# Kernel tuning notes

Hardware: AMD Instinct MI355X
Metric: run time of the kernel (lower is better)

The kernel has to match this reference:

```python
import jax, jax.numpy as jnp
import numpy as np

N = 50000
F_IN = 128
E = 800000
C = 32      # hidden_channels
H1 = 8      # heads_1
H2 = 1      # heads_2
NEG_SLOPE = 0.2


def setup_inputs() -> dict:
    key = jax.random.key(0)
    ks = jax.random.split(key, 16)
    s = 0.1
    x = jax.random.normal(ks[0], (N, F_IN), dtype=jnp.float32)
    edge_index = jax.random.randint(ks[1], (2, E), 0, N, dtype=jnp.int32)
    # layer 1: in=F_IN, out=C, heads=H1, concat=True
    Wl1 = jax.random.normal(ks[2], (H1 * C, F_IN), dtype=jnp.float32) * s
    bl1 = jnp.zeros((H1 * C,), dtype=jnp.float32)
    Wr1 = jax.random.normal(ks[3], (H1 * C, F_IN), dtype=jnp.float32) * s
    br1 = jnp.zeros((H1 * C,), dtype=jnp.float32)
    att1 = jax.random.normal(ks[4], (H1, C), dtype=jnp.float32) * s
    bias1 = jnp.zeros((H1 * C,), dtype=jnp.float32)
    # layer 2: in=H1*C, out=C, heads=H2, concat=False (mean)
    Wl2 = jax.random.normal(ks[5], (H2 * C, H1 * C), dtype=jnp.float32) * s
    bl2 = jnp.zeros((H2 * C,), dtype=jnp.float32)
    Wr2 = jax.random.normal(ks[6], (H2 * C, H1 * C), dtype=jnp.float32) * s
    br2 = jnp.zeros((H2 * C,), dtype=jnp.float32)
    att2 = jax.random.normal(ks[7], (H2, C), dtype=jnp.float32) * s
    bias2 = jnp.zeros((C,), dtype=jnp.float32)
    return {"x": x, "edge_index": edge_index,
            "Wl1": Wl1, "bl1": bl1, "Wr1": Wr1, "br1": br1, "att1": att1, "bias1": bias1,
            "Wl2": Wl2, "bl2": bl2, "Wr2": Wr2, "br2": br2, "att2": att2, "bias2": bias2}


def _gatv2_layer(x, src, dst, Wl, bl, Wr, br, att, bias, heads, out_c, concat):
    n = x.shape[0]
    xl = (x @ Wl.T + bl).reshape(n, heads, out_c)  # source transform
    xr = (x @ Wr.T + br).reshape(n, heads, out_c)  # target transform
    z = jax.nn.leaky_relu(xl[src] + xr[dst], NEG_SLOPE)          # [E, H, C]
    logit = jnp.einsum('ehc,hc->eh', z, att)                     # [E, H]
    # segment softmax over incoming edges of each target node
    m = jax.ops.segment_max(logit, dst, num_segments=n)          # [N, H]
    ex = jnp.exp(logit - m[dst])
    denom = jax.ops.segment_sum(ex, dst, num_segments=n)
    alpha = ex / jnp.maximum(denom[dst], 1e-16)                  # [E, H]
    out = jax.ops.segment_sum(alpha[..., None] * xl[src], dst, num_segments=n)  # [N, H, C]
    out = out.reshape(n, heads * out_c) if concat else out.mean(axis=1)
    return out + bias


def reference(x, edge_index, Wl1, bl1, Wr1, br1, att1, bias1,
              Wl2, bl2, Wr2, br2, att2, bias2):
    n = x.shape[0]
    # PyG GATv2Conv default: add self loops
    loops = jnp.arange(n, dtype=edge_index.dtype)
    src = jnp.concatenate([edge_index[0], loops])
    dst = jnp.concatenate([edge_index[1], loops])
    h = _gatv2_layer(x, src, dst, Wl1, bl1, Wr1, br1, att1, bias1, H1, C, True)
    h = jax.nn.gelu(h, approximate=False)
    out = _gatv2_layer(h, src, dst, Wl2, bl2, Wr2, br2, att2, bias2, H2, C, False)
    return out
```

## Files before the change

kernel.cpp:

```cpp
#include <hip/hip_runtime.h>
#include <hip/hip_bf16.h>


typedef unsigned short u16;
typedef short bf16x8 __attribute__((ext_vector_type(8)));
typedef float f32x4 __attribute__((ext_vector_type(4)));
typedef float f32x2 __attribute__((ext_vector_type(2)));

#define F_IN   128
#define CH     32
#define H1     8
#define JT1    512
#define JH1    256
#define JT2    64
#define JH2    32

#define OFF_Y1     0UL
#define OFF_H      52000000UL
#define OFF_Y2     78000000UL
#define OFF_COL    85000000UL
#define OFF_DEG    89000000UL
#define OFF_ROW    89400000UL
#define OFF_CUR    89800000UL
#define OFF_WC     90200000UL
#define OFF_FLAG   90600000UL
#define OFF_BSUM   90700000UL
#define WS_NEED    91000000UL

#define W_WL1   0
#define W_BL1   32768
#define W_WR1   33024
#define W_BR1   65792
#define W_ATT1  66048
#define W_BIAS1 66304
#define W_WL2   66560
#define W_BL2   74752
#define W_WR2   74784
#define W_BR2   82976
#define W_ATT2  83008
#define W_BIAS2 83040
#define W_TOTAL 83072

__device__ inline float b2f(u16 u) { return __uint_as_float(((unsigned)u) << 16); }
__device__ inline u16 f2b(float f) {
    unsigned u = __float_as_uint(f);
    unsigned r = (u + 0x7fffu + ((u >> 16) & 1u)) >> 16;
    return (u16)r;
}
__device__ inline unsigned cvtpk(float lo, float hi) {
    unsigned r;
    asm("v_cvt_pk_bf16_f32 %0, %1, %2" : "=v"(r) : "v"(lo), "v"(hi));
    return r;
}
__device__ inline f32x2 pk_add(f32x2 a, f32x2 b) {
    f32x2 d;
    asm("v_pk_add_f32 %0, %1, %2" : "=v"(d) : "v"(a), "v"(b));
    return d;
}
__device__ inline f32x2 pk_mul(f32x2 a, f32x2 b) {
    f32x2 d;
    asm("v_pk_mul_f32 %0, %1, %2" : "=v"(d) : "v"(a), "v"(b));
    return d;
}
__device__ inline f32x2 pk_fma(f32x2 a, f32x2 b, f32x2 c) {
    f32x2 d;
    asm("v_pk_fma_f32 %0, %1, %2, %3" : "=v"(d) : "v"(a), "v"(b), "v"(c));
    return d;
}
__device__ inline f32x2 unpk(unsigned u) {
    f32x2 d;
    d.x = __uint_as_float(u << 16);
    d.y = __uint_as_float(u & 0xffff0000u);
    return d;
}
__device__ inline f32x2 pabs(f32x2 z) {
    f32x2 d;
    d.x = __uint_as_float(__float_as_uint(z.x) & 0x7fffffffu);
    d.y = __uint_as_float(__float_as_uint(z.y) & 0x7fffffffu);
    return d;
}

struct WcArgs { const void* src[12]; int cum[13]; };

__global__ __launch_bounds__(256) void prep(
    WcArgs a, const u16* __restrict__ xprobe, u16* __restrict__ dst, int total,
    int* __restrict__ flagOut, int NBW,
    const int* __restrict__ ei, int* __restrict__ deg, int E_, int NP) {
    const int t = threadIdx.x;
    if ((int)blockIdx.x >= NBW) {
        int e = ((int)blockIdx.x - NBW) * 256 + t;
        if (e >= E_ + NP) return;
        int dstn = (e < E_) ? ei[E_ + e] : e - E_;
        atomicAdd(deg + dstn, 1);
        return;
    }
    __shared__ int cnt[256];
    __shared__ int sflag;
    int c = 0;
    for (int i = t; i < 512; i += 256) {
        u16 u = xprobe[i];
        int e = (u >> 7) & 0xff;
        c += (u == 0 || (e >= 100 && e <= 141)) ? 1 : 0;
    }
    cnt[t] = c; __syncthreads();
    for (int off = 128; off; off >>= 1) {
        if (t < off) cnt[t] += cnt[t + off];
        __syncthreads();
    }
    if (t == 0) {
        sflag = (cnt[0] >= 440) ? 1 : 0;
        if (blockIdx.x == 0) *flagOut = sflag;
    }
    __syncthreads();
    const int fl = sflag;
    int i = blockIdx.x * 256 + t;
    if (i >= total) return;
    int s = 0;
    while (i >= a.cum[s + 1]) s++;
    int rel = i - a.cum[s];
    if (fl) dst[i] = ((const u16*)a.src[s])[rel];
    else    dst[i] = f2b(((const float*)a.src[s])[rel]);
}

__global__ __launch_bounds__(256) void scan_part(const int* __restrict__ deg,
                                                 int* __restrict__ bsum, int NN) {
    __shared__ int red[256];
    int b = blockIdx.x, t = threadIdx.x;
    int base = b * 1024 + t * 4;
    int s = 0;
#pragma unroll
    for (int j = 0; j < 4; j++) { int i = base + j; if (i < NN) s += deg[i]; }
    red[t] = s; __syncthreads();
    for (int off = 128; off; off >>= 1) {
        if (t < off) red[t] += red[t + off];
        __syncthreads();
    }
    if (t == 0) bsum[b] = red[0];
}

__global__ __launch_bounds__(256) void scan_final(
    const int* __restrict__ deg, const int* __restrict__ bsum,
    int* __restrict__ rowptr, int* __restrict__ cur, int NN, int NB) {
    __shared__ int sb[256];
    __shared__ int ps[256];
    int b = blockIdx.x, t = threadIdx.x;
    int bv = (t < NB) ? bsum[t] : 0;
    sb[t] = bv; __syncthreads();
    for (int off = 1; off < 256; off <<= 1) {
        int x = (t >= off) ? sb[t - off] : 0;
        __syncthreads();
        sb[t] += x;
        __syncthreads();
    }
    if (b == 0 && t == 0) rowptr[NN] = sb[NB - 1];
    int boff = (b == 0) ? 0 : sb[b - 1];

    int base = b * 1024 + t * 4;
    int v[4]; int s = 0;
#pragma unroll
    for (int j = 0; j < 4; j++) { int i = base + j; v[j] = (i < NN) ? deg[i] : 0; s += v[j]; }
    ps[t] = s; __syncthreads();
    for (int off = 1; off < 256; off <<= 1) {
        int x = (t >= off) ? ps[t - off] : 0;
        __syncthreads();
        ps[t] += x;
        __syncthreads();
    }
    int run = boff + (t ? ps[t - 1] : 0);
#pragma unroll
    for (int j = 0; j < 4; j++) {
        int i = base + j;
        if (i < NN) { rowptr[i] = run; cur[i] = run; run += v[j]; }
    }
}

template <int K, int NG, bool DYN>
__device__ __forceinline__ void gemm_body(
    float (*cs)[32][68],
    const void* __restrict__ X, const u16* __restrict__ Wl, const u16* __restrict__ Wr,
    const u16* __restrict__ bl, const u16* __restrict__ br,
    u16* __restrict__ Y, int M, int JH, const int* __restrict__ flagp, int bm0) {
    const int t = threadIdx.x, w = t >> 6, l = t & 63;
    const int JT = 2 * JH;
    const int lr = l & 15, lk = (l >> 4) * 8;
    const int fl = DYN ? *flagp : 1;

    int rowm[2];
#pragma unroll
    for (int mt = 0; mt < 2; mt++) {
        int row = bm0 + w * 32 + mt * 16 + lr;
        if (row >= M) row = M - 1;
        rowm[mt] = row;
    }

    constexpr int KK = K / 32;
    bf16x8 afr[2][KK];
    if (fl) {
        const u16* xb = (const u16*)X;
#pragma unroll
        for (int mt = 0; mt < 2; mt++)
#pragma unroll
            for (int kk = 0; kk < KK; kk++)
                afr[mt][kk] = *(const bf16x8*)(xb + (size_t)rowm[mt] * K + lk + kk * 32);
    } else {
        const float* xf = (const float*)X;
#pragma unroll
        for (int mt = 0; mt < 2; mt++)
#pragma unroll
            for (int kk = 0; kk < KK; kk++) {
                const float* p = xf + (size_t)rowm[mt] * K + lk + kk * 32;
                float4 v0 = *(const float4*)p;
                float4 v1 = *(const float4*)(p + 4);
                uint4 o;
                o.x = cvtpk(v0.x, v0.y); o.y = cvtpk(v0.z, v0.w);
                o.z = cvtpk(v1.x, v1.y); o.w = cvtpk(v1.z, v1.w);
                afr[mt][kk] = *(bf16x8*)&o;
            }
    }

#pragma unroll 1
    for (int g = 0; g < NG; g++) {
        const int bn0 = g * 64;
        const u16* bx[4];
        float bv[4];
#pragma unroll
        for (int nt = 0; nt < 4; nt++) {
            int j = bn0 + nt * 16 + lr;
            const u16* wp = (j < JH) ? (Wl + (size_t)j * K) : (Wr + (size_t)(j - JH) * K);
            bx[nt] = wp + lk;
            bv[nt] = b2f(j < JH ? bl[j] : br[j - JH]);
        }

        f32x4 acc[2][4];
#pragma unroll
        for (int mt = 0; mt < 2; mt++)
#pragma unroll
            for (int nt = 0; nt < 4; nt++) acc[mt][nt] = (f32x4){0.f, 0.f, 0.f, 0.f};

#pragma unroll
        for (int kk = 0; kk < KK; kk++) {
            bf16x8 b[4];
#pragma unroll
            for (int nt = 0; nt < 4; nt++) b[nt] = *(const bf16x8*)(bx[nt] + kk * 32);
#pragma unroll
            for (int mt = 0; mt < 2; mt++)
#pragma unroll
                for (int nt = 0; nt < 4; nt++)
                    acc[mt][nt] = __builtin_amdgcn_mfma_f32_16x16x32_bf16(
                        afr[mt][kk], b[nt], acc[mt][nt], 0, 0, 0);
        }

#pragma unroll
        for (int mt = 0; mt < 2; mt++)
#pragma unroll
            for (int nt = 0; nt < 4; nt++)
#pragma unroll
                for (int r = 0; r < 4; r++)
                    cs[w][mt * 16 + (l >> 4) * 4 + r][nt * 16 + lr] = acc[mt][nt][r] + bv[nt];

#pragma unroll
        for (int p = 0; p < 4; p++) {
            int rl = p * 8 + (l >> 3);
            int grow = bm0 + w * 32 + rl;
            if (grow < M) {
                const float* rp = &cs[w][rl][(l & 7) * 8];
                float4 v0 = *(const float4*)rp;
                float4 v1 = *(const float4*)(rp + 4);
                uint4 o;
                o.x = cvtpk(v0.x, v0.y); o.y = cvtpk(v0.z, v0.w);
                o.z = cvtpk(v1.x, v1.y); o.w = cvtpk(v1.z, v1.w);
                *(uint4*)(Y + (size_t)grow * JT + bn0 + (l & 7) * 8) = o;
            }
        }
    }
}

__global__ __launch_bounds__(256) void gemm1_scatter(
    const void* __restrict__ X, const u16* __restrict__ Wl, const u16* __restrict__ Wr,
    const u16* __restrict__ bl, const u16* __restrict__ br,
    u16* __restrict__ Y, int M, const int* __restrict__ flagp, int NBG,
    const int* __restrict__ ei, int* __restrict__ cur, int* __restrict__ col,
    int E_, int NP) {
    __shared__ float cs[4][32][68];
    if ((int)blockIdx.x < NBG) {
        gemm_body<F_IN, 8, true>(cs, X, Wl, Wr, bl, br, Y, M, JH1, flagp,
                                 (int)blockIdx.x * 128);
        return;
    }
    int e = ((int)blockIdx.x - NBG) * 256 + threadIdx.x;
    if (e >= E_ + NP) return;
    int src, dst;
    if (e < E_) { src = ei[e]; dst = ei[E_ + e]; }
    else        { src = dst = e - E_; }
    int pos = atomicAdd(cur + dst, 1);
    col[pos] = src;
}

__global__ __launch_bounds__(256) void gemm2_k(
    const u16* __restrict__ X, const u16* __restrict__ Wl, const u16* __restrict__ Wr,
    const u16* __restrict__ bl, const u16* __restrict__ br,
    u16* __restrict__ Y, int M, const int* __restrict__ flagp) {
    __shared__ float cs[4][32][68];
    gemm_body<JH1, 1, false>(cs, X, Wl, Wr, bl, br, Y, M, JH2, flagp,
                             (int)blockIdx.x * 128);
}

__global__ __launch_bounds__(256, 4) void agg1(
    const u16* __restrict__ Y1, const int* __restrict__ rowptr,
    const int* __restrict__ col, const u16* __restrict__ att,
    const u16* __restrict__ bias, u16* __restrict__ hout, int NN) {
    const int wid = blockIdx.x * 4 + (threadIdx.x >> 6);
    if (wid >= NN) return;
    const int lane = threadIdx.x & 63, half = lane >> 5, hl = lane & 31;
    const int n = wid;

    f32x2 xr2[4], a06[4], a04[4];
    {
        uint4 rx = *(const uint4*)(Y1 + (size_t)n * JT1 + JH1 + hl * 8);
        uint4 ra = *(const uint4*)(att + hl * 8);
        unsigned ux[4] = {rx.x, rx.y, rx.z, rx.w};
        unsigned ua[4] = {ra.x, ra.y, ra.z, ra.w};
#pragma unroll
        for (int p = 0; p < 4; p++) {
            xr2[p] = unpk(ux[p]);
            f32x2 a = unpk(ua[p]);
            a06[p].x = 0.6f * a.x; a06[p].y = 0.6f * a.y;
            a04[p].x = 0.4f * a.x; a04[p].y = 0.4f * a.y;
        }
    }
    f32x2 acc2[4] = {{0.f,0.f},{0.f,0.f},{0.f,0.f},{0.f,0.f}};
    float dsum = 0.f;

    auto edge = [&](uint4 raw) {
        unsigned uw[4] = {raw.x, raw.y, raw.z, raw.w};
        f32x2 xl2[4];
        f32x2 p2 = {0.f, 0.f};
#pragma unroll
        for (int p = 0; p < 4; p++) {
            xl2[p] = unpk(uw[p]);
            f32x2 z = pk_add(xl2[p], xr2[p]);
            p2 = pk_fma(z, a06[p], p2);
            p2 = pk_fma(pabs(z), a04[p], p2);
        }
        float pl = p2.x + p2.y;
        pl += __shfl_xor(pl, 1); pl += __shfl_xor(pl, 2);
        float e = __expf(pl);
        dsum += e;
        f32x2 e2; e2.x = e; e2.y = e;
#pragma unroll
        for (int p = 0; p < 4; p++) acc2[p] = pk_fma(e2, xl2[p], acc2[p]);
    };

    const int beg = rowptr[n], end = rowptr[n + 1];
    int i = beg + half;
    for (; i + 14 < end; i += 16) {
        int s[8];
#pragma unroll
        for (int k = 0; k < 8; k++) s[k] = col[i + 2 * k];
        uint4 r[8];
#pragma unroll
        for (int k = 0; k < 8; k++) r[k] = *(const uint4*)(Y1 + (size_t)s[k] * JT1 + hl * 8);
#pragma unroll
        for (int k = 0; k < 8; k++) edge(r[k]);
    }
    for (; i + 6 < end; i += 8) {
        int s0 = col[i], s1 = col[i + 2], s2 = col[i + 4], s3 = col[i + 6];
        uint4 r0 = *(const uint4*)(Y1 + (size_t)s0 * JT1 + hl * 8);
        uint4 r1 = *(const uint4*)(Y1 + (size_t)s1 * JT1 + hl * 8);
        uint4 r2 = *(const uint4*)(Y1 + (size_t)s2 * JT1 + hl * 8);
        uint4 r3 = *(const uint4*)(Y1 + (size_t)s3 * JT1 + hl * 8);
        edge(r0); edge(r1); edge(r2); edge(r3);
    }
    for (; i < end; i += 2) {
        uint4 r0 = *(const uint4*)(Y1 + (size_t)col[i] * JT1 + hl * 8);
        edge(r0);
    }

    dsum += __shfl_xor(dsum, 32);
#pragma unroll
    for (int p = 0; p < 4; p++) {
        acc2[p].x += __shfl_xor(acc2[p].x, 32);
        acc2[p].y += __shfl_xor(acc2[p].y, 32);
    }

    if (half == 0) {
        float inv = 1.f / fmaxf(dsum, 1e-16f);
        u16 bu[8];
        *(uint4*)bu = *(const uint4*)(bias + hl * 8);
        float v[8];
#pragma unroll
        for (int p = 0; p < 4; p++) {
            float x0 = acc2[p].x * inv + b2f(bu[2 * p]);
            float x1 = acc2[p].y * inv + b2f(bu[2 * p + 1]);
            v[2 * p]     = 0.5f * x0 * (1.f + erff(x0 * 0.70710678118654752f));
            v[2 * p + 1] = 0.5f * x1 * (1.f + erff(x1 * 0.70710678118654752f));
        }
        uint4 o;
        o.x = cvtpk(v[0], v[1]); o.y = cvtpk(v[2], v[3]);
        o.z = cvtpk(v[4], v[5]); o.w = cvtpk(v[6], v[7]);
        *(uint4*)(hout + (size_t)n * JH1 + hl * 8) = o;
    }
}

__global__ __launch_bounds__(256) void agg2(
    const u16* __restrict__ Y2, const int* __restrict__ rowptr,
    const int* __restrict__ col, const u16* __restrict__ att,
    const u16* __restrict__ bias, void* __restrict__ dout, int NN,
    const int* __restrict__ flag) {
    const int wid = blockIdx.x * 4 + (threadIdx.x >> 6);
    if (wid >= NN) return;
    const int lane = threadIdx.x & 63, le = lane >> 4, cl = lane & 15;
    const int n = wid;

    f32x2 xr2 = unpk(*(const unsigned*)(Y2 + (size_t)n * JT2 + JH2 + cl * 2));
    f32x2 av  = unpk(*(const unsigned*)(att + cl * 2));
    f32x2 a06; a06.x = 0.6f * av.x; a06.y = 0.6f * av.y;
    f32x2 a04; a04.x = 0.4f * av.x; a04.y = 0.4f * av.y;
    f32x2 acc2 = {0.f, 0.f};
    float dsum = 0.f;

    auto edge = [&](unsigned raw, bool act) {
        f32x2 xl2 = unpk(raw);
        f32x2 z = pk_add(xl2, xr2);
        f32x2 p2 = pk_fma(z, a06, (f32x2){0.f, 0.f});
        p2 = pk_fma(pabs(z), a04, p2);
        float pl = p2.x + p2.y;
        pl += __shfl_xor(pl, 1); pl += __shfl_xor(pl, 2);
        pl += __shfl_xor(pl, 4); pl += __shfl_xor(pl, 8);
        float e = __expf(pl);
        if (!act) e = 0.f;
        dsum += e;
        f32x2 e2; e2.x = e; e2.y = e;
        acc2 = pk_fma(e2, xl2, acc2);
    };

    const int beg = rowptr[n], end = rowptr[n + 1];
    int i = beg;
    for (; i + 16 <= end; i += 16) {
        int s0 = col[i + le], s1 = col[i + 4 + le];
        int s2 = col[i + 8 + le], s3 = col[i + 12 + le];
        unsigned r0 = *(const unsigned*)(Y2 + (size_t)s0 * JT2 + cl * 2);
        unsigned r1 = *(const unsigned*)(Y2 + (size_t)s1 * JT2 + cl * 2);
        unsigned r2 = *(const unsigned*)(Y2 + (size_t)s2 * JT2 + cl * 2);
        unsigned r3 = *(const unsigned*)(Y2 + (size_t)s3 * JT2 + cl * 2);
        edge(r0, true); edge(r1, true); edge(r2, true); edge(r3, true);
    }
    for (; i + 8 <= end; i += 8) {
        int sA = col[i + le];
        int sB = col[i + 4 + le];
        unsigned rA = *(const unsigned*)(Y2 + (size_t)sA * JT2 + cl * 2);
        unsigned rB = *(const unsigned*)(Y2 + (size_t)sB * JT2 + cl * 2);
        edge(rA, true);
        edge(rB, true);
    }
    for (; i < end; i += 4) {
        int idx = i + le;
        bool act = idx < end;
        int s0 = col[act ? idx : end - 1];
        unsigned r0 = *(const unsigned*)(Y2 + (size_t)s0 * JT2 + cl * 2);
        edge(r0, act);
    }

    dsum += __shfl_xor(dsum, 16); dsum += __shfl_xor(dsum, 32);
    acc2.x += __shfl_xor(acc2.x, 16); acc2.x += __shfl_xor(acc2.x, 32);
    acc2.y += __shfl_xor(acc2.y, 16); acc2.y += __shfl_xor(acc2.y, 32);

    if (le == 0) {
        float inv = 1.f / fmaxf(dsum, 1e-16f);
        f32x2 bv = unpk(*(const unsigned*)(bias + cl * 2));
        float v0 = acc2.x * inv + bv.x;
        float v1 = acc2.y * inv + bv.y;
        if (*flag) {
            *(unsigned*)((u16*)dout + n * JH2 + cl * 2) = cvtpk(v0, v1);
        } else {
            float2 o; o.x = v0; o.y = v1;
            *(float2*)((float*)dout + n * JH2 + cl * 2) = o;
        }
    }
}

extern "C" void kernel_launch(void* const* d_in, const int* in_sizes, int n_in,
                              void* d_out, int out_size, void* d_ws, size_t ws_size,
                              hipStream_t stream) {
    const int NN = in_sizes[0] / F_IN;
    const int EE = in_sizes[1] / 2;
    const int EP = EE + NN;
    if (ws_size < WS_NEED) return;

    char* w = (char*)d_ws;
    u16*   Y1   = (u16*)(w + OFF_Y1);
    u16*   hbuf = (u16*)(w + OFF_H);
    u16*   Y2   = (u16*)(w + OFF_Y2);
    int*   col  = (int*)(w + OFF_COL);
    int*   deg  = (int*)(w + OFF_DEG);
    int*   rowp = (int*)(w + OFF_ROW);
    int*   cur  = (int*)(w + OFF_CUR);
    u16*   Wc   = (u16*)(w + OFF_WC);
    int*   flag = (int*)(w + OFF_FLAG);
    int*   bsum = (int*)(w + OFF_BSUM);

    const int* ei = (const int*)d_in[1];

    hipMemsetAsync(deg, 0, (size_t)NN * 4, stream);
    {
        WcArgs a;
        int sizes[12] = {JH1 * F_IN, JH1, JH1 * F_IN, JH1, H1 * CH, JH1,
                         JH2 * JH1, JH2, JH2 * JH1, JH2, JH2, JH2};
        int c = 0;
        for (int s = 0; s < 12; s++) { a.src[s] = d_in[2 + s]; a.cum[s] = c; c += sizes[s]; }
        a.cum[12] = c;
        const int NBW = (W_TOTAL + 255) / 256;
        const int NBE = (EP + 255) / 256;
        prep<<<NBW + NBE, 256, 0, stream>>>(a, (const u16*)d_in[0], Wc, W_TOTAL,
                                            flag, NBW, ei, deg, EE, NN);
    }

    const int NB = (NN + 1023) / 1024;
    scan_part<<<NB, 256, 0, stream>>>(deg, bsum, NN);
    scan_final<<<NB, 256, 0, stream>>>(deg, bsum, rowp, cur, NN, NB);

    {
        const int NBG = (NN + 127) / 128;
        const int NBE = (EP + 255) / 256;
        gemm1_scatter<<<NBG + NBE, 256, 0, stream>>>(
            d_in[0], Wc + W_WL1, Wc + W_WR1, Wc + W_BL1, Wc + W_BR1,
            Y1, NN, flag, NBG, ei, cur, col, EE, NN);
    }
    agg1<<<(NN + 3) / 4, 256, 0, stream>>>(Y1, rowp, col, Wc + W_ATT1,
                                           Wc + W_BIAS1, hbuf, NN);

    gemm2_k<<<(NN + 127) / 128, 256, 0, stream>>>(
        hbuf, Wc + W_WL2, Wc + W_WR2, Wc + W_BL2, Wc + W_BR2, Y2, NN, flag);
    agg2<<<(NN + 3) / 4, 256, 0, stream>>>(Y2, rowp, col, Wc + W_ATT2,
                                           Wc + W_BIAS2, d_out, NN, flag);
}
```

Baseline: 242.0 us.

## Process nodes in degree-sorted order in aggregation kernels for load balance

Builds a histogram of node in-degrees during the scan and prefix-sums it. A new kernel scatters node ids into a degree-sorted permutation, which agg1 and agg2 use to map waves to nodes. The aim is to group nodes of similar in-degree into the same blocks and reduce imbalance from uneven edge counts. The cost is an extra kernel, atomics, and loss of contiguous node access for the self-feature reads and output writes.

```diff
diff --git a/kernel.cpp b/kernel.cpp
--- a/kernel.cpp
+++ b/kernel.cpp
@@ -19,7 +19,10 @@
 #define OFF_H      52000000UL
 #define OFF_Y2     78000000UL
 #define OFF_COL    85000000UL
+#define OFF_PERM   88400000UL
 #define OFF_DEG    89000000UL
+#define OFF_DH     89200000UL
+#define OFF_DCUR   89201024UL
 #define OFF_ROW    89400000UL
 #define OFF_CUR    89800000UL
 #define OFF_WC     90200000UL
@@ -123,24 +126,37 @@
 }
 
 __global__ __launch_bounds__(256) void scan_part(const int* __restrict__ deg,
-                                                 int* __restrict__ bsum, int NN) {
+                                                 int* __restrict__ bsum,
+                                                 int* __restrict__ dh, int NN) {
     __shared__ int red[256];
+    __shared__ int lh[256];
     int b = blockIdx.x, t = threadIdx.x;
+    lh[t] = 0;
     int base = b * 1024 + t * 4;
     int s = 0;
-#pragma unroll
-    for (int j = 0; j < 4; j++) { int i = base + j; if (i < NN) s += deg[i]; }
+    __syncthreads();
+#pragma unroll
+    for (int j = 0; j < 4; j++) {
+        int i = base + j;
+        if (i < NN) {
+            int v = deg[i];
+            s += v;
+            atomicAdd(&lh[v < 255 ? v : 255], 1);
+        }
+    }
     red[t] = s; __syncthreads();
     for (int off = 128; off; off >>= 1) {
         if (t < off) red[t] += red[t + off];
         __syncthreads();
     }
     if (t == 0) bsum[b] = red[0];
+    if (lh[t]) atomicAdd(dh + t, lh[t]);
 }
 
 __global__ __launch_bounds__(256) void scan_final(
     const int* __restrict__ deg, const int* __restrict__ bsum,
-    int* __restrict__ rowptr, int* __restrict__ cur, int NN, int NB) {
+    int* __restrict__ rowptr, int* __restrict__ cur, int NN, int NB,
+    const int* __restrict__ dh, int* __restrict__ dcur) {
     __shared__ int sb[256];
     __shared__ int ps[256];
     int b = blockIdx.x, t = threadIdx.x;
@@ -172,6 +188,28 @@
         int i = base + j;
         if (i < NN) { rowptr[i] = run; cur[i] = run; run += v[j]; }
     }
+
+    if (b == 0) {
+        __syncthreads();
+        int dv = dh[t];
+        sb[t] = dv; __syncthreads();
+        for (int off = 1; off < 256; off <<= 1) {
+            int x = (t >= off) ? sb[t - off] : 0;
+            __syncthreads();
+            sb[t] += x;
+            __syncthreads();
+        }
+        dcur[t] = sb[t] - dv;
+    }
+}
+
+__global__ void dsort_scatter(const int* __restrict__ deg, int* __restrict__ dcur,
+                              int* __restrict__ perm, int NN) {
+    int i = blockIdx.x * 256 + threadIdx.x;
+    if (i >= NN) return;
+    int v = deg[i];
+    int pos = atomicAdd(dcur + (v < 255 ? v : 255), 1);
+    perm[pos] = i;
 }
 
 template <int K, int NG, bool DYN>
@@ -308,11 +346,12 @@
 __global__ __launch_bounds__(256, 4) void agg1(
     const u16* __restrict__ Y1, const int* __restrict__ rowptr,
     const int* __restrict__ col, const u16* __restrict__ att,
-    const u16* __restrict__ bias, u16* __restrict__ hout, int NN) {
+    const u16* __restrict__ bias, u16* __restrict__ hout, int NN,
+    const int* __restrict__ perm) {
     const int wid = blockIdx.x * 4 + (threadIdx.x >> 6);
     if (wid >= NN) return;
     const int lane = threadIdx.x & 63, half = lane >> 5, hl = lane & 31;
-    const int n = wid;
+    const int n = perm[wid];
 
     f32x2 xr2[4], a06[4], a04[4];
     {
@@ -406,11 +445,11 @@
     const u16* __restrict__ Y2, const int* __restrict__ rowptr,
     const int* __restrict__ col, const u16* __restrict__ att,
     const u16* __restrict__ bias, void* __restrict__ dout, int NN,
-    const int* __restrict__ flag) {
+    const int* __restrict__ flag, const int* __restrict__ perm) {
     const int wid = blockIdx.x * 4 + (threadIdx.x >> 6);
     if (wid >= NN) return;
     const int lane = threadIdx.x & 63, le = lane >> 4, cl = lane & 15;
-    const int n = wid;
+    const int n = perm[wid];
 
     f32x2 xr2 = unpk(*(const unsigned*)(Y2 + (size_t)n * JT2 + JH2 + cl * 2));
     f32x2 av  = unpk(*(const unsigned*)(att + cl * 2));
@@ -492,7 +531,10 @@
     u16*   hbuf = (u16*)(w + OFF_H);
     u16*   Y2   = (u16*)(w + OFF_Y2);
     int*   col  = (int*)(w + OFF_COL);
+    int*   perm = (int*)(w + OFF_PERM);
     int*   deg  = (int*)(w + OFF_DEG);
+    int*   dh   = (int*)(w + OFF_DH);
+    int*   dcur = (int*)(w + OFF_DCUR);
     int*   rowp = (int*)(w + OFF_ROW);
     int*   cur  = (int*)(w + OFF_CUR);
     u16*   Wc   = (u16*)(w + OFF_WC);
@@ -501,7 +543,7 @@
 
     const int* ei = (const int*)d_in[1];
 
-    hipMemsetAsync(deg, 0, (size_t)NN * 4, stream);
+    hipMemsetAsync(deg, 0, (size_t)NN * 4 + 2048, stream);
     {
         WcArgs a;
         int sizes[12] = {JH1 * F_IN, JH1, JH1 * F_IN, JH1, H1 * CH, JH1,
@@ -516,8 +558,9 @@
     }
 
     const int NB = (NN + 1023) / 1024;
-    scan_part<<<NB, 256, 0, stream>>>(deg, bsum, NN);
-    scan_final<<<NB, 256, 0, stream>>>(deg, bsum, rowp, cur, NN, NB);
+    scan_part<<<NB, 256, 0, stream>>>(deg, bsum, dh, NN);
+    scan_final<<<NB, 256, 0, stream>>>(deg, bsum, rowp, cur, NN, NB, dh, dcur);
+    dsort_scatter<<<(NN + 255) / 256, 256, 0, stream>>>(deg, dcur, perm, NN);
 
     {
         const int NBG = (NN + 127) / 128;
@@ -527,10 +570,10 @@
             Y1, NN, flag, NBG, ei, cur, col, EE, NN);
     }
     agg1<<<(NN + 3) / 4, 256, 0, stream>>>(Y1, rowp, col, Wc + W_ATT1,
-                                           Wc + W_BIAS1, hbuf, NN);
+                                           Wc + W_BIAS1, hbuf, NN, perm);
 
     gemm2_k<<<(NN + 127) / 128, 256, 0, stream>>>(
         hbuf, Wc + W_WL2, Wc + W_WR2, Wc + W_BL2, Wc + W_BR2, Y2, NN, flag);
     agg2<<<(NN + 3) / 4, 256, 0, stream>>>(Y2, rowp, col, Wc + W_ATT2,
-                                           Wc + W_BIAS2, d_out, NN, flag);
-}
+                                           Wc + W_BIAS2, d_out, NN, flag, perm);
+}
```

Result: slower. 382.7 us (+58.1%).
